# Kernel optimization log

Hardware: AMD Instinct MI355X
Metric: run time of the kernel (lower is better)

The kernel has to match this reference:

```python
import jax, jax.numpy as jnp
import numpy as np

FDS = [80, 160, 400, 600]
N, E, G, IN = 20000, 320000, 128, 3072
EPS = 1e-5  # BatchNorm1d default eps


def setup_inputs():
    key = jax.random.key(0)
    ks = iter(jax.random.split(key, 64))
    inp = {}
    inp["x"] = jax.random.normal(next(ks), (N, IN), jnp.float32)
    inp["edge_index"] = jax.random.randint(next(ks), (2, E), 0, N)
    inp["batch"] = jnp.sort(jax.random.randint(next(ks), (N,), 0, G))
    for i, fd in enumerate(FDS):
        din = IN if i == 0 else FDS[i - 1]
        def u(shape, fan):
            s = 1.0 / np.sqrt(fan)
            return jax.random.uniform(next(ks), shape, jnp.float32, -s, s)
        inp[f"wa{i}"] = u((din, 4 * fd), din)      # Linear(din, 4*fd)
        inp[f"ba{i}"] = u((4 * fd,), din)
        inp[f"wb{i}"] = u((4 * fd, fd), 4 * fd)    # Linear(4*fd, fd)
        inp[f"bb{i}"] = u((fd,), 4 * fd)
        inp[f"gw{i}"] = u((fd, fd), fd)            # GCNConv weight
        inp[f"gb{i}"] = jnp.zeros((fd,), jnp.float32)  # GCNConv bias
        inp[f"gamma{i}"] = jnp.ones((fd,), jnp.float32)
        inp[f"beta{i}"] = jnp.zeros((fd,), jnp.float32)
        inp[f"mean{i}"] = jax.random.normal(next(ks), (fd,), jnp.float32) * 0.1
        inp[f"var{i}"] = jax.random.uniform(next(ks), (fd,), jnp.float32, 0.5, 1.5)
    return inp


def _gcn_edges(edge_index, n):
    # GCNConv default: add self-loops, symmetric D^-1/2 (A+I) D^-1/2 normalization
    loops = jnp.arange(n)
    src = jnp.concatenate([edge_index[0], loops])
    dst = jnp.concatenate([edge_index[1], loops])
    deg = jax.ops.segment_sum(jnp.ones(src.shape, jnp.float32), dst, num_segments=n)
    dinv = jnp.where(deg > 0, jax.lax.rsqrt(deg), 0.0)
    return src, dst, dinv[src] * dinv[dst]


def _forward(x, edge_index, batch, params):
    src, dst, norm = _gcn_edges(edge_index, N)
    for (wa, ba, wb, bb, gw, gb, gamma, beta, mean, var) in params:
        h = jax.nn.relu(x @ wa + ba)   # dropout = identity in eval mode
        h = jax.nn.relu(h @ wb + bb)
        h = h @ gw                     # GCN linear transform
        # gather -> normalize -> scatter-add message passing, then bias
        h = jax.ops.segment_sum(h[src] * norm[:, None], dst, num_segments=N) + gb
        # BatchNorm1d (eval: running stats)
        h = (h - mean) * jax.lax.rsqrt(var + EPS) * gamma + beta
        x = jax.nn.relu(h)             # residual branch is dead: dims never match
    return jax.ops.segment_max(x, batch, num_segments=G)  # global_max_pool


def reference(x, edge_index, batch,
              wa0, ba0, wb0, bb0, gw0, gb0, gamma0, beta0, mean0, var0,
              wa1, ba1, wb1, bb1, gw1, gb1, gamma1, beta1, mean1, var1,
              wa2, ba2, wb2, bb2, gw2, gb2, gamma2, beta2, mean2, var2,
              wa3, ba3, wb3, bb3, gw3, gb3, gamma3, beta3, mean3, var3):
    params = [
        (wa0, ba0, wb0, bb0, gw0, gb0, gamma0, beta0, mean0, var0),
        (wa1, ba1, wb1, bb1, gw1, gb1, gamma1, beta1, mean1, var1),
        (wa2, ba2, wb2, bb2, gw2, gb2, gamma2, beta2, mean2, var2),
        (wa3, ba3, wb3, bb3, gw3, gb3, gamma3, beta3, mean3, var3),
    ]
    return _forward(x, edge_index, batch, params)
```

## Files before the change

kernel.cpp:

```cpp
#include <hip/hip_runtime.h>
#include <cstdint>
#include <cstddef>
#include <cmath>


#define EPS_BN 1e-5f

typedef unsigned short u16;
typedef short short8 __attribute__((ext_vector_type(8)));
typedef u16 u16x8 __attribute__((ext_vector_type(8)));
typedef u16 u16x4 __attribute__((ext_vector_type(4)));
typedef float fx4 __attribute__((ext_vector_type(4)));

__device__ __forceinline__ u16 bf16_rn(float f) {
  unsigned u = __float_as_uint(f);
  return (u16)((u + 0x7FFFu + ((u >> 16) & 1u)) >> 16);
}
__device__ __forceinline__ float bf16_f(u16 h) {
  return __uint_as_float(((unsigned)h) << 16);
}

__device__ __forceinline__ void gload16(const void* g, void* l) {
  __builtin_amdgcn_global_load_lds(
      (const __attribute__((address_space(1))) void*)g,
      (__attribute__((address_space(3))) void*)l, 16, 0, 0);
}

__device__ __forceinline__ void map_tile(int b, int tm, int tn, int T,
                                         int& mt, int& nt) {
  const int x = b & 7;
  const int s = b >> 3;
  const int cap = ((tm - x + 7) >> 3) * tn;
  if (s < cap) {
    const int q = s / tn;
    mt = x + (q << 3);
    nt = s - q * tn;
    return;
  }
  int r = s - cap;
  for (int xp = 0; xp < x; ++xp) {
    const int nbp = (T - xp + 7) >> 3;
    const int capp = ((tm - xp + 7) >> 3) * tn;
    if (nbp > capp) r += nbp - capp;
  }
  for (int xq = 0; xq < 8; ++xq) {
    const int nbq = (T - xq + 7) >> 3;
    const int capq = ((tm - xq + 7) >> 3) * tn;
    const int def = capq - nbq;
    if (def > 0) {
      if (r < def) {
        const int sq = nbq + r;
        const int q = sq / tn;
        mt = xq + (q << 3);
        nt = sq - q * tn;
        return;
      }
      r -= def;
    }
  }
  mt = 0; nt = 0;
}

template <int OUTMODE, bool SPLITA>
__global__ __launch_bounds__(256, 2) void gemm_mfma(
    const u16* __restrict__ Ahi, const u16* __restrict__ Alo,
    const float* __restrict__ Af,
    const u16* __restrict__ Bhi, const u16* __restrict__ Blo,
    const float* __restrict__ bias,
    float* __restrict__ Cf, u16* __restrict__ Chi, u16* __restrict__ Clo,
    int M, int N, int K, int lda, int ldb, int ldc, int tm, int tn) {
  __shared__ __align__(16) u16 As[2][128 * 32];
  __shared__ __align__(16) u16 Bs[2][128 * 32];

  int mt, nt;
  map_tile(blockIdx.x, tm, tn, tm * tn, mt, nt);
  const int m0 = mt * 128;
  const int n0 = nt * 128;

  const int tid = threadIdx.x;
  const int lane = tid & 63;
  const int wid = tid >> 6;
  const int wm = (wid >> 1) * 64;
  const int wn = (wid & 1) * 64;
  const int quad = lane >> 4;
  const int l15 = lane & 15;

  const int srow = tid >> 2;
  const int sg = ((tid & 3) ^ srow) & 3;
  int ar0 = m0 + srow;      if (ar0 >= M) ar0 = M - 1;
  int ar1 = m0 + srow + 64; if (ar1 >= M) ar1 = M - 1;
  int br0 = n0 + srow;      if (br0 >= N) br0 = N - 1;
  int br1 = n0 + srow + 64; if (br1 >= N) br1 = N - 1;
  const size_t aof0 = (size_t)ar0 * lda + (sg << 3);
  const size_t aof1 = (size_t)ar1 * lda + (sg << 3);
  const size_t bof0 = (size_t)br0 * ldb + (sg << 3);
  const size_t bof1 = (size_t)br1 * ldb + (sg << 3);
  const int l0 = wid << 9;
  const int l1 = 2048 + (wid << 9);
  const int wls = srow * 32 + ((tid & 3) << 3);

  fx4 zf = {0.f, 0.f, 0.f, 0.f};
  fx4 acc[4][4];
#pragma unroll
  for (int a = 0; a < 4; ++a)
#pragma unroll
    for (int b = 0; b < 4; ++b) acc[a][b] = zf;

  const int nk = (K + 31) >> 5;
  for (int ki = 0; ki < nk; ++ki) {
    const int k0 = ki << 5;
    u16x8 va_h[2], va_l[2];
    if (SPLITA) {
#pragma unroll
      for (int it = 0; it < 2; ++it) {
        const float* pp = Af + (it ? aof1 : aof0) + k0;
        const fx4 f0 = *(const fx4*)pp;
        const fx4 f1 = *(const fx4*)(pp + 4);
        u16x8 h, l;
#pragma unroll
        for (int j = 0; j < 4; ++j) {
          const u16 hb = bf16_rn(f0[j]);
          h[j] = hb;
          l[j] = bf16_rn(f0[j] - bf16_f(hb));
        }
#pragma unroll
        for (int j = 0; j < 4; ++j) {
          const u16 hb = bf16_rn(f1[j]);
          h[4 + j] = hb;
          l[4 + j] = bf16_rn(f1[j] - bf16_f(hb));
        }
        va_h[it] = h;
        va_l[it] = l;
      }
    }

    if (ki) __syncthreads();

    if (SPLITA) {
      gload16(Bhi + bof0 + k0, &Bs[0][l0]);
      gload16(Bhi + bof1 + k0, &Bs[0][l1]);
      gload16(Blo + bof0 + k0, &Bs[1][l0]);
      gload16(Blo + bof1 + k0, &Bs[1][l1]);
      *(u16x8*)&As[0][wls] = va_h[0];
      *(u16x8*)&As[0][wls + 2048] = va_h[1];
      *(u16x8*)&As[1][wls] = va_l[0];
      *(u16x8*)&As[1][wls + 2048] = va_l[1];
    } else {
      gload16(Ahi + aof0 + k0, &As[0][l0]);
      gload16(Ahi + aof1 + k0, &As[0][l1]);
      gload16(Alo + aof0 + k0, &As[1][l0]);
      gload16(Alo + aof1 + k0, &As[1][l1]);
      gload16(Bhi + bof0 + k0, &Bs[0][l0]);
      gload16(Bhi + bof1 + k0, &Bs[0][l1]);
      gload16(Blo + bof0 + k0, &Bs[1][l0]);
      gload16(Blo + bof1 + k0, &Bs[1][l1]);
    }
    __syncthreads();

    short8 ah[4], al[4], bh[4], bl[4];
#pragma unroll
    for (int t = 0; t < 4; ++t) {
      const int rA = wm + t * 16 + l15;
      const int oa = rA * 32 + (((quad ^ rA) & 3) << 3);
      ah[t] = *(const short8*)&As[0][oa];
      al[t] = *(const short8*)&As[1][oa];
      const int rB = wn + t * 16 + l15;
      const int ob = rB * 32 + (((quad ^ rB) & 3) << 3);
      bh[t] = *(const short8*)&Bs[0][ob];
      bl[t] = *(const short8*)&Bs[1][ob];
    }
#pragma unroll
    for (int a = 0; a < 4; ++a)
#pragma unroll
      for (int b = 0; b < 4; ++b) {
        acc[a][b] = __builtin_amdgcn_mfma_f32_16x16x32_bf16(ah[a], bh[b], acc[a][b], 0, 0, 0);
        acc[a][b] = __builtin_amdgcn_mfma_f32_16x16x32_bf16(ah[a], bl[b], acc[a][b], 0, 0, 0);
        acc[a][b] = __builtin_amdgcn_mfma_f32_16x16x32_bf16(al[a], bh[b], acc[a][b], 0, 0, 0);
      }
  }

#pragma unroll
  for (int a = 0; a < 4; ++a)
#pragma unroll
    for (int b = 0; b < 4; ++b) {
      const int gn = n0 + wn + b * 16 + l15;
      if (gn >= ldc) continue;
      const bool live = gn < N;
      const float bv = (OUTMODE == 1 && live) ? bias[gn] : 0.f;
#pragma unroll
      for (int r = 0; r < 4; ++r) {
        const int gm = m0 + wm + a * 16 + quad * 4 + r;
        if (gm >= M) continue;
        float v = live ? acc[a][b][r] : 0.f;
        if (OUTMODE == 1) {
          v = live ? fmaxf(v + bv, 0.f) : 0.f;
          const u16 hb = bf16_rn(v);
          Chi[(size_t)gm * ldc + gn] = hb;
          Clo[(size_t)gm * ldc + gn] = bf16_rn(v - bf16_f(hb));
        } else {
          Cf[(size_t)gm * ldc + gn] = v;
        }
      }
    }
}

struct TSJob { const float* W; u16* Th; u16* Tl; int K; int Kp; int N; int tiles_k; int base; };
struct TSJobs { TSJob j[12]; };

__global__ __launch_bounds__(256) void transpose_split_all(TSJobs jobs, int njobs) {
  const int b = blockIdx.x;
  int ji = 0;
  while (ji + 1 < njobs && jobs.j[ji + 1].base <= b) ++ji;
  const TSJob J = jobs.j[ji];
  const int t = b - J.base;
  const int k0 = (t % J.tiles_k) * 32;
  const int n0 = (t / J.tiles_k) * 32;
  __shared__ float tile[32][33];
  const int tx = threadIdx.x & 31, ty = threadIdx.x >> 5;
#pragma unroll
  for (int i = 0; i < 32; i += 8) {
    const int k = k0 + ty + i, n = n0 + tx;
    tile[ty + i][tx] = (k < J.K && n < J.N) ? J.W[(size_t)k * J.N + n] : 0.f;
  }
  __syncthreads();
#pragma unroll
  for (int i = 0; i < 32; i += 8) {
    const int n = n0 + ty + i, k = k0 + tx;
    if (n < J.N && k < J.Kp) {
      const float f = tile[tx][ty + i];
      const u16 hb = bf16_rn(f);
      J.Th[(size_t)n * J.Kp + k] = hb;
      J.Tl[(size_t)n * J.Kp + k] = bf16_rn(f - bf16_f(hb));
    }
  }
}

__global__ void count_deg(const int* __restrict__ dst, int E, int* __restrict__ cnt) {
  int e = blockIdx.x * blockDim.x + threadIdx.x;
  if (e < E) atomicAdd(&cnt[dst[e]], 1);
}

__global__ void compute_dinv(const int* __restrict__ cnt, float* __restrict__ dinv, int N) {
  int i = blockIdx.x * blockDim.x + threadIdx.x;
  if (i < N) dinv[i] = rsqrtf((float)(cnt[i] + 1));
}

__global__ void scan_block(const int* __restrict__ cnt, int* __restrict__ partial,
                           int* __restrict__ blocksum, int N) {
  __shared__ int s[256];
  const int t = threadIdx.x;
  const int i = blockIdx.x * 256 + t;
  int v = (i < N) ? cnt[i] : 0;
  s[t] = v;
  __syncthreads();
  for (int off = 1; off < 256; off <<= 1) {
    int u = (t >= off) ? s[t - off] : 0;
    __syncthreads();
    s[t] += u;
    __syncthreads();
  }
  if (i < N) partial[i] = s[t];
  if (t == 255) blocksum[blockIdx.x] = s[255];
}

__global__ void scan_sums(int* __restrict__ blocksum, int NB) {
  __shared__ int s[256];
  const int t = threadIdx.x;
  int v = (t < NB) ? blocksum[t] : 0;
  s[t] = v;
  __syncthreads();
  for (int off = 1; off < 256; off <<= 1) {
    int u = (t >= off) ? s[t - off] : 0;
    __syncthreads();
    s[t] += u;
    __syncthreads();
  }
  if (t < NB) blocksum[t] = s[t] - v;
}

__global__ void finalize_rowptr(const int* __restrict__ partial, const int* __restrict__ blockoff,
                                int* __restrict__ rowptr, int N) {
  int i = blockIdx.x * 256 + threadIdx.x;
  if (i < N) rowptr[i + 1] = partial[i] + blockoff[blockIdx.x];
  if (i == 0) rowptr[0] = 0;
}

__global__ void fill_csr(const int* __restrict__ src, const int* __restrict__ dst, int E,
                         const int* __restrict__ rowptr, int* __restrict__ cursor,
                         int* __restrict__ colidx) {
  int e = blockIdx.x * blockDim.x + threadIdx.x;
  if (e < E) {
    int d = dst[e];
    int p = atomicAdd(&cursor[d], 1);
    colidx[rowptr[d] + p] = src[e];
  }
}

__global__ void mp_bn_relu(
    const float* __restrict__ H, const int* __restrict__ rowptr,
    const int* __restrict__ colidx, const float* __restrict__ dinv,
    const float* __restrict__ gb, const float* __restrict__ gamma,
    const float* __restrict__ beta, const float* __restrict__ mean,
    const float* __restrict__ var,
    u16* __restrict__ Xh, u16* __restrict__ Xl, int N, int F, int Fp) {
  const int nch = Fp >> 2;
  const int idx = blockIdx.x * blockDim.x + threadIdx.x;
  if (idx >= N * nch) return;
  const int i = idx / nch;
  const int c = idx - i * nch;
  const size_t rowi = (size_t)i * Fp + (c << 2);
  if ((c << 2) >= F) {
    const u16x4 z = {0, 0, 0, 0};
    *(u16x4*)(Xh + rowi) = z;
    *(u16x4*)(Xl + rowi) = z;
    return;
  }
  const float di = dinv[i];
  fx4 acc = (di * di) * *(const fx4*)(H + rowi);
  const int e0 = rowptr[i], e1 = rowptr[i + 1];
  int e = e0;
  for (; e + 4 <= e1; e += 4) {
    const int s0 = colidx[e + 0], s1 = colidx[e + 1];
    const int s2 = colidx[e + 2], s3 = colidx[e + 3];
    const float w0 = di * dinv[s0], w1 = di * dinv[s1];
    const float w2 = di * dinv[s2], w3 = di * dinv[s3];
    const fx4 v0 = *(const fx4*)(H + (size_t)s0 * Fp + (c << 2));
    const fx4 v1 = *(const fx4*)(H + (size_t)s1 * Fp + (c << 2));
    const fx4 v2 = *(const fx4*)(H + (size_t)s2 * Fp + (c << 2));
    const fx4 v3 = *(const fx4*)(H + (size_t)s3 * Fp + (c << 2));
    acc += w0 * v0;
    acc += w1 * v1;
    acc += w2 * v2;
    acc += w3 * v3;
  }
  for (; e < e1; ++e) {
    const int s = colidx[e];
    acc += (di * dinv[s]) * *(const fx4*)(H + (size_t)s * Fp + (c << 2));
  }
  u16x4 oh, ol;
#pragma unroll
  for (int j = 0; j < 4; ++j) {
    const int col = (c << 2) + j;
    float v = (acc[j] + gb[col] - mean[col]) * rsqrtf(var[col] + EPS_BN) * gamma[col] + beta[col];
    v = fmaxf(v, 0.f);
    const u16 hb = bf16_rn(v);
    oh[j] = hb;
    ol[j] = bf16_rn(v - bf16_f(hb));
  }
  *(u16x4*)(Xh + rowi) = oh;
  *(u16x4*)(Xl + rowi) = ol;
}

__global__ void pool_seg(const u16* __restrict__ Xh, const u16* __restrict__ Xl,
                         const int* __restrict__ batch, float* __restrict__ out,
                         int N, int F, int ldx) {
  const int g = blockIdx.x;
  int lo = 0, hi = N;
  while (lo < hi) { int m = (lo + hi) >> 1; if (batch[m] < g) lo = m + 1; else hi = m; }
  const int s0 = lo;
  hi = N;
  while (lo < hi) { int m = (lo + hi) >> 1; if (batch[m] <= g) lo = m + 1; else hi = m; }
  const int s1 = lo;
  const int c = threadIdx.x;
  if (c * 4 >= F) return;
  fx4 mx = {-INFINITY, -INFINITY, -INFINITY, -INFINITY};
  for (int i = s0; i < s1; ++i) {
    const size_t off = (size_t)i * ldx + (c << 2);
    const u16x4 h = *(const u16x4*)(Xh + off);
    const u16x4 l = *(const u16x4*)(Xl + off);
#pragma unroll
    for (int j = 0; j < 4; ++j) mx[j] = fmaxf(mx[j], bf16_f(h[j]) + bf16_f(l[j]));
  }
  *(fx4*)(out + (size_t)g * F + (c << 2)) = mx;
}

extern "C" void kernel_launch(void* const* d_in, const int* in_sizes, int n_in,
                              void* d_out, int out_size, void* d_ws, size_t ws_size,
                              hipStream_t stream) {
  const float* x = (const float*)d_in[0];
  const int* edges = (const int*)d_in[1];
  const int* batch = (const int*)d_in[2];
  const int E = in_sizes[1] / 2;
  const int Nn = in_sizes[2];

  static const int FDS[4]  = {80, 160, 400, 600};
  static const int FDP[4]  = {96, 160, 416, 608};
  static const int DINS[4] = {3072, 80, 160, 400};
  static const int DINP[4] = {3072, 96, 160, 416};
  const float *wa[4], *ba[4], *wb[4], *bb[4], *gw[4], *gb[4], *gamma[4], *beta[4], *mean[4], *var[4];
  for (int i = 0; i < 4; ++i) {
    const int b = 3 + 10 * i;
    wa[i] = (const float*)d_in[b + 0];
    ba[i] = (const float*)d_in[b + 1];
    wb[i] = (const float*)d_in[b + 2];
    bb[i] = (const float*)d_in[b + 3];
    gw[i] = (const float*)d_in[b + 4];
    gb[i] = (const float*)d_in[b + 5];
    gamma[i] = (const float*)d_in[b + 6];
    beta[i] = (const float*)d_in[b + 7];
    mean[i] = (const float*)d_in[b + 8];
    var[i] = (const float*)d_in[b + 9];
  }

  char* p = (char*)d_ws;
  auto alloc = [&](size_t bytes) {
    char* r = p;
    p += (bytes + 255) & ~(size_t)255;
    return r;
  };
  u16* actA_h = (u16*)alloc((size_t)Nn * 2400 * 2);
  u16* actA_l = (u16*)alloc((size_t)Nn * 2400 * 2);
  u16* actB_h = (u16*)alloc((size_t)Nn * 608 * 2);
  u16* actB_l = (u16*)alloc((size_t)Nn * 608 * 2);
  float* H3 = (float*)actA_h;

  u16 *waT_h[4], *waT_l[4], *wbT_h[4], *wbT_l[4], *gwT_h[4], *gwT_l[4];
  for (int i = 0; i < 4; ++i) {
    const size_t s1 = (size_t)4 * FDS[i] * DINP[i];
    const size_t s2 = (size_t)FDS[i] * 4 * FDS[i];
    const size_t s3 = (size_t)FDS[i] * FDP[i];
    waT_h[i] = (u16*)alloc(s1 * 2);
    waT_l[i] = (u16*)alloc(s1 * 2);
    wbT_h[i] = (u16*)alloc(s2 * 2);
    wbT_l[i] = (u16*)alloc(s2 * 2);
    gwT_h[i] = (u16*)alloc(s3 * 2);
    gwT_l[i] = (u16*)alloc(s3 * 2);
  }

  int* cnt = (int*)alloc((size_t)Nn * sizeof(int));
  int* cursor = (int*)alloc((size_t)Nn * sizeof(int));
  int* partial = (int*)alloc((size_t)Nn * sizeof(int));
  int* blocksum = (int*)alloc(256 * sizeof(int));
  int* rowptr = (int*)alloc((size_t)(Nn + 1) * sizeof(int));
  int* colidx = (int*)alloc((size_t)E * sizeof(int));
  float* dinv = (float*)alloc((size_t)Nn * sizeof(float));

  const int* srcIdx = edges;
  const int* dstIdx = edges + E;

  {
    TSJobs jobs;
    int base = 0, ji = 0;
    auto addjob = [&](const float* W, int K, int Kp, int Ncols, u16* Th, u16* Tl) {
      const int tk = Kp / 32, tn = (Ncols + 31) / 32;
      jobs.j[ji++] = TSJob{W, Th, Tl, K, Kp, Ncols, tk, base};
      base += tk * tn;
    };
    for (int i = 0; i < 4; ++i) {
      addjob(wa[i], DINS[i], DINP[i], 4 * FDS[i], waT_h[i], waT_l[i]);
      addjob(wb[i], 4 * FDS[i], 4 * FDS[i], FDS[i], wbT_h[i], wbT_l[i]);
      addjob(gw[i], FDS[i], FDP[i], FDS[i], gwT_h[i], gwT_l[i]);
    }
    transpose_split_all<<<base, 256, 0, stream>>>(jobs, 12);
  }

  hipMemsetAsync(cnt, 0, (size_t)Nn * sizeof(int), stream);
  hipMemsetAsync(cursor, 0, (size_t)Nn * sizeof(int), stream);

  const int EB = (E + 255) / 256;
  const int NB = (Nn + 255) / 256;
  count_deg<<<EB, 256, 0, stream>>>(dstIdx, E, cnt);
  compute_dinv<<<NB, 256, 0, stream>>>(cnt, dinv, Nn);
  scan_block<<<NB, 256, 0, stream>>>(cnt, partial, blocksum, Nn);
  scan_sums<<<1, 256, 0, stream>>>(blocksum, NB);
  finalize_rowptr<<<NB, 256, 0, stream>>>(partial, blocksum, rowptr, Nn);
  fill_csr<<<EB, 256, 0, stream>>>(srcIdx, dstIdx, E, rowptr, cursor, colidx);

  const int tm = (Nn + 127) / 128;
  for (int i = 0; i < 4; ++i) {
    const int fd = FDS[i], fdp = FDP[i];
    const int hid = 4 * fd;
    const int din = DINS[i], dinp = DINP[i];

    {
      const int tn = (hid + 127) / 128;
      if (i == 0) {
        gemm_mfma<1, true><<<tm * tn, 256, 0, stream>>>(
            nullptr, nullptr, x, waT_h[0], waT_l[0], ba[0],
            nullptr, actA_h, actA_l, Nn, hid, din, din, dinp, hid, tm, tn);
      } else {
        gemm_mfma<1, false><<<tm * tn, 256, 0, stream>>>(
            actB_h, actB_l, nullptr, waT_h[i], waT_l[i], ba[i],
            nullptr, actA_h, actA_l, Nn, hid, din, dinp, dinp, hid, tm, tn);
      }
    }
    {
      const int tn = (fd + 127) / 128;
      gemm_mfma<1, false><<<tm * tn, 256, 0, stream>>>(
          actA_h, actA_l, nullptr, wbT_h[i], wbT_l[i], bb[i],
          nullptr, actB_h, actB_l, Nn, fd, hid, hid, hid, fdp, tm, tn);
    }
    {
      const int tn = (fd + 127) / 128;
      gemm_mfma<0, false><<<tm * tn, 256, 0, stream>>>(
          actB_h, actB_l, nullptr, gwT_h[i], gwT_l[i], nullptr,
          H3, nullptr, nullptr, Nn, fd, fd, fdp, fdp, fdp, tm, tn);
    }
    {
      const int items = Nn * (fdp >> 2);
      mp_bn_relu<<<(items + 255) / 256, 256, 0, stream>>>(
          H3, rowptr, colidx, dinv, gb[i], gamma[i], beta[i], mean[i], var[i],
          actB_h, actB_l, Nn, fd, fdp);
    }
  }

  pool_seg<<<out_size / 600, 192, 0, stream>>>(actB_h, actB_l, batch, (float*)d_out,
                                               Nn, 600, 608);
}
```

Before: 1.682 ms.

## Double-buffer LDS tiles in MFMA GEMM to overlap next-tile loads with compute

Doubles the shared-memory A/B staging buffers and adds a prologue load. Each iteration now prefetches tile k+1 into the alternate buffer while MFMAs run on the current one, with one barrier per iteration instead of two. In split-A mode the fp32 A values are loaded early and converted to hi/lo bf16 after the MFMAs. LDS usage doubles to 64KB per block, which may limit the two-blocks-per-CU occupancy the launch bounds target. Register pressure also rises from holding the prefetched A values.

```diff
diff --git a/kernel.cpp b/kernel.cpp
--- a/kernel.cpp
+++ b/kernel.cpp
@@ -69,8 +69,8 @@
     const float* __restrict__ bias,
     float* __restrict__ Cf, u16* __restrict__ Chi, u16* __restrict__ Clo,
     int M, int N, int K, int lda, int ldb, int ldc, int tm, int tn) {
-  __shared__ __align__(16) u16 As[2][128 * 32];
-  __shared__ __align__(16) u16 Bs[2][128 * 32];
+  __shared__ __align__(16) u16 As[2][2][128 * 32];
+  __shared__ __align__(16) u16 Bs[2][2][128 * 32];
 
   int mt, nt;
   map_tile(blockIdx.x, tm, tn, tm * tn, mt, nt);
@@ -107,67 +107,86 @@
     for (int b = 0; b < 4; ++b) acc[a][b] = zf;
 
   const int nk = (K + 31) >> 5;
+
+  if (SPLITA) {
+    gload16(Bhi + bof0, &Bs[0][0][l0]);
+    gload16(Bhi + bof1, &Bs[0][0][l1]);
+    gload16(Blo + bof0, &Bs[0][1][l0]);
+    gload16(Blo + bof1, &Bs[0][1][l1]);
+#pragma unroll
+    for (int it = 0; it < 2; ++it) {
+      const float* pp = Af + (it ? aof1 : aof0);
+      const fx4 f0 = *(const fx4*)pp;
+      const fx4 f1 = *(const fx4*)(pp + 4);
+      u16x8 h, l;
+#pragma unroll
+      for (int j = 0; j < 4; ++j) {
+        const u16 hb = bf16_rn(f0[j]);
+        h[j] = hb;
+        l[j] = bf16_rn(f0[j] - bf16_f(hb));
+      }
+#pragma unroll
+      for (int j = 0; j < 4; ++j) {
+        const u16 hb = bf16_rn(f1[j]);
+        h[4 + j] = hb;
+        l[4 + j] = bf16_rn(f1[j] - bf16_f(hb));
+      }
+      *(u16x8*)&As[0][0][wls + it * 2048] = h;
+      *(u16x8*)&As[0][1][wls + it * 2048] = l;
+    }
+  } else {
+    gload16(Ahi + aof0, &As[0][0][l0]);
+    gload16(Ahi + aof1, &As[0][0][l1]);
+    gload16(Alo + aof0, &As[0][1][l0]);
+    gload16(Alo + aof1, &As[0][1][l1]);
+    gload16(Bhi + bof0, &Bs[0][0][l0]);
+    gload16(Bhi + bof1, &Bs[0][0][l1]);
+    gload16(Blo + bof0, &Bs[0][1][l0]);
+    gload16(Blo + bof1, &Bs[0][1][l1]);
+  }
+
   for (int ki = 0; ki < nk; ++ki) {
-    const int k0 = ki << 5;
-    u16x8 va_h[2], va_l[2];
-    if (SPLITA) {
-#pragma unroll
-      for (int it = 0; it < 2; ++it) {
-        const float* pp = Af + (it ? aof1 : aof0) + k0;
-        const fx4 f0 = *(const fx4*)pp;
-        const fx4 f1 = *(const fx4*)(pp + 4);
-        u16x8 h, l;
-#pragma unroll
-        for (int j = 0; j < 4; ++j) {
-          const u16 hb = bf16_rn(f0[j]);
-          h[j] = hb;
-          l[j] = bf16_rn(f0[j] - bf16_f(hb));
-        }
-#pragma unroll
-        for (int j = 0; j < 4; ++j) {
-          const u16 hb = bf16_rn(f1[j]);
-          h[4 + j] = hb;
-          l[4 + j] = bf16_rn(f1[j] - bf16_f(hb));
-        }
-        va_h[it] = h;
-        va_l[it] = l;
-      }
-    }
-
-    if (ki) __syncthreads();
-
-    if (SPLITA) {
-      gload16(Bhi + bof0 + k0, &Bs[0][l0]);
-      gload16(Bhi + bof1 + k0, &Bs[0][l1]);
-      gload16(Blo + bof0 + k0, &Bs[1][l0]);
-      gload16(Blo + bof1 + k0, &Bs[1][l1]);
-      *(u16x8*)&As[0][wls] = va_h[0];
-      *(u16x8*)&As[0][wls + 2048] = va_h[1];
-      *(u16x8*)&As[1][wls] = va_l[0];
-      *(u16x8*)&As[1][wls + 2048] = va_l[1];
-    } else {
-      gload16(Ahi + aof0 + k0, &As[0][l0]);
-      gload16(Ahi + aof1 + k0, &As[0][l1]);
-      gload16(Alo + aof0 + k0, &As[1][l0]);
-      gload16(Alo + aof1 + k0, &As[1][l1]);
-      gload16(Bhi + bof0 + k0, &Bs[0][l0]);
-      gload16(Bhi + bof1 + k0, &Bs[0][l1]);
-      gload16(Blo + bof0 + k0, &Bs[1][l0]);
-      gload16(Blo + bof1 + k0, &Bs[1][l1]);
-    }
+    const int cur = ki & 1;
     __syncthreads();
+
+    const bool pre = (ki + 1) < nk;
+    const int kn = (ki + 1) << 5;
+    fx4 pA0 = zf, pA1 = zf, pA2 = zf, pA3 = zf;
+    if (pre) {
+      if (SPLITA) {
+        gload16(Bhi + bof0 + kn, &Bs[cur ^ 1][0][l0]);
+        gload16(Bhi + bof1 + kn, &Bs[cur ^ 1][0][l1]);
+        gload16(Blo + bof0 + kn, &Bs[cur ^ 1][1][l0]);
+        gload16(Blo + bof1 + kn, &Bs[cur ^ 1][1][l1]);
+        const float* pp0 = Af + aof0 + kn;
+        const float* pp1 = Af + aof1 + kn;
+        pA0 = *(const fx4*)pp0;
+        pA1 = *(const fx4*)(pp0 + 4);
+        pA2 = *(const fx4*)pp1;
+        pA3 = *(const fx4*)(pp1 + 4);
+      } else {
+        gload16(Ahi + aof0 + kn, &As[cur ^ 1][0][l0]);
+        gload16(Ahi + aof1 + kn, &As[cur ^ 1][0][l1]);
+        gload16(Alo + aof0 + kn, &As[cur ^ 1][1][l0]);
+        gload16(Alo + aof1 + kn, &As[cur ^ 1][1][l1]);
+        gload16(Bhi + bof0 + kn, &Bs[cur ^ 1][0][l0]);
+        gload16(Bhi + bof1 + kn, &Bs[cur ^ 1][0][l1]);
+        gload16(Blo + bof0 + kn, &Bs[cur ^ 1][1][l0]);
+        gload16(Blo + bof1 + kn, &Bs[cur ^ 1][1][l1]);
+      }
+    }
 
     short8 ah[4], al[4], bh[4], bl[4];
 #pragma unroll
     for (int t = 0; t < 4; ++t) {
       const int rA = wm + t * 16 + l15;
       const int oa = rA * 32 + (((quad ^ rA) & 3) << 3);
-      ah[t] = *(const short8*)&As[0][oa];
-      al[t] = *(const short8*)&As[1][oa];
+      ah[t] = *(const short8*)&As[cur][0][oa];
+      al[t] = *(const short8*)&As[cur][1][oa];
       const int rB = wn + t * 16 + l15;
       const int ob = rB * 32 + (((quad ^ rB) & 3) << 3);
-      bh[t] = *(const short8*)&Bs[0][ob];
-      bl[t] = *(const short8*)&Bs[1][ob];
+      bh[t] = *(const short8*)&Bs[cur][0][ob];
+      bl[t] = *(const short8*)&Bs[cur][1][ob];
     }
 #pragma unroll
     for (int a = 0; a < 4; ++a)
@@ -177,6 +196,39 @@
         acc[a][b] = __builtin_amdgcn_mfma_f32_16x16x32_bf16(ah[a], bl[b], acc[a][b], 0, 0, 0);
         acc[a][b] = __builtin_amdgcn_mfma_f32_16x16x32_bf16(al[a], bh[b], acc[a][b], 0, 0, 0);
       }
+
+    if (SPLITA && pre) {
+      u16x8 h0, l0v, h1, l1v;
+#pragma unroll
+      for (int j = 0; j < 4; ++j) {
+        u16 hb = bf16_rn(pA0[j]);
+        h0[j] = hb;
+        l0v[j] = bf16_rn(pA0[j] - bf16_f(hb));
+      }
+#pragma unroll
+      for (int j = 0; j < 4; ++j) {
+        u16 hb = bf16_rn(pA1[j]);
+        h0[4 + j] = hb;
+        l0v[4 + j] = bf16_rn(pA1[j] - bf16_f(hb));
+      }
+#pragma unroll
+      for (int j = 0; j < 4; ++j) {
+        u16 hb = bf16_rn(pA2[j]);
+        h1[j] = hb;
+        l1v[j] = bf16_rn(pA2[j] - bf16_f(hb));
+      }
+#pragma unroll
+      for (int j = 0; j < 4; ++j) {
+        u16 hb = bf16_rn(pA3[j]);
+        h1[4 + j] = hb;
+        l1v[4 + j] = bf16_rn(pA3[j] - bf16_f(hb));
+      }
+      const int nb = cur ^ 1;
+      *(u16x8*)&As[nb][0][wls] = h0;
+      *(u16x8*)&As[nb][1][wls] = l0v;
+      *(u16x8*)&As[nb][0][wls + 2048] = h1;
+      *(u16x8*)&As[nb][1][wls + 2048] = l1v;
+    }
   }
 
 #pragma unroll
```

New measurement: 1.797 ms. 1.07x slower.
